# Kernel tuning notes

Measured on AMD Instinct MI355X. Metric: run time of the kernel, lower is better.

The kernel has to match this reference:

```python
import jax, jax.numpy as jnp
import numpy as np

N = 100000
D = 64
FE = 8
E = 1600000


def setup_inputs() -> dict:
    key = jax.random.key(0)
    ks = jax.random.split(key, 24)
    s = 0.05
    inp = {
        "H_adapted_t": jax.random.normal(ks[0], (N, D), jnp.float32),
        "event_vector": jax.random.normal(ks[1], (N, FE), jnp.float32),
        "edge_index": jax.random.randint(ks[2], (2, E), 0, N, jnp.int32),
        # event encoder MLP
        "enc_W1": jax.random.normal(ks[3], (FE, D), jnp.float32) * s,
        "enc_b1": jnp.zeros((D,), jnp.float32),
        "enc_W2": jax.random.normal(ks[4], (D, D), jnp.float32) * s,
        "enc_b2": jnp.zeros((D,), jnp.float32),
        # GCNConv
        "gcn_W": jax.random.normal(ks[5], (D, D), jnp.float32) * s,
        "gcn_b": jnp.zeros((D,), jnp.float32),
        # GATConv (heads=1, concat=False)
        "gat_W": jax.random.normal(ks[6], (D, D), jnp.float32) * s,
        "gat_att_src": jax.random.normal(ks[7], (D,), jnp.float32) * s,
        "gat_att_dst": jax.random.normal(ks[8], (D,), jnp.float32) * s,
        "gat_b": jnp.zeros((D,), jnp.float32),
        # gate fusion
        "gate_W": jax.random.normal(ks[9], (2 * D, D), jnp.float32) * s,
        "gate_b": jnp.zeros((D,), jnp.float32),
        # residual decoder
        "res_W1": jax.random.normal(ks[10], (2 * D, D), jnp.float32) * s,
        "res_b1": jnp.zeros((D,), jnp.float32),
        "res_W2": jax.random.normal(ks[11], (D, D), jnp.float32) * s,
        "res_b2": jnp.zeros((D,), jnp.float32),
        # speed head
        "sp_W1": jax.random.normal(ks[12], (D, 32), jnp.float32) * s,
        "sp_b1": jnp.zeros((32,), jnp.float32),
        "sp_W2": jax.random.normal(ks[13], (32, 1), jnp.float32) * s,
        "sp_b2": jnp.zeros((1,), jnp.float32),
    }
    return inp


def _gcn(x, src, dst, W, b, n):
    # PyG GCNConv: x' = D^{-1/2} (A + I) D^{-1/2} X W + b
    h = x @ W
    deg = jax.ops.segment_sum(jnp.ones_like(dst, jnp.float32), dst, num_segments=n)
    dinv = jnp.where(deg > 0, jax.lax.rsqrt(jnp.maximum(deg, 1e-12)), 0.0)
    norm = dinv[src] * dinv[dst]  # [E+N]
    out = jax.ops.segment_sum(h[src] * norm[:, None], dst, num_segments=n)
    return out + b


def _gat(x, src, dst, W, att_src, att_dst, b, n):
    # PyG GATConv (1 head): alpha = softmax_dst(leaky_relu(a_s.Wx_src + a_d.Wx_dst))
    h = x @ W
    a_s = h @ att_src  # [n]
    a_d = h @ att_dst
    e = jax.nn.leaky_relu(a_s[src] + a_d[dst], negative_slope=0.2)  # [E+N]
    m = jax.ops.segment_max(e, dst, num_segments=n)
    ex = jnp.exp(e - m[dst])
    z = jax.ops.segment_sum(ex, dst, num_segments=n)
    alpha = ex / z[dst]
    out = jax.ops.segment_sum(h[src] * alpha[:, None], dst, num_segments=n)
    return out + b


def reference(H_adapted_t, event_vector, edge_index,
              enc_W1, enc_b1, enc_W2, enc_b2,
              gcn_W, gcn_b,
              gat_W, gat_att_src, gat_att_dst, gat_b,
              gate_W, gate_b,
              res_W1, res_b1, res_W2, res_b2,
              sp_W1, sp_b1, sp_W2, sp_b2):
    n = H_adapted_t.shape[0]
    # add self-loops (PyG default for both convs)
    loop = jnp.arange(n, dtype=edge_index.dtype)
    src = jnp.concatenate([edge_index[0], loop])
    dst = jnp.concatenate([edge_index[1], loop])

    # event encoder
    emb = jax.nn.relu(event_vector @ enc_W1 + enc_b1) @ enc_W2 + enc_b2
    # diffusion: GCN -> ReLU -> GAT -> ReLU
    x = jax.nn.relu(_gcn(emb, src, dst, gcn_W, gcn_b, n))
    diffused = jax.nn.relu(_gat(x, src, dst, gat_W, gat_att_src, gat_att_dst, gat_b, n))

    fusion = jnp.concatenate([H_adapted_t, diffused], axis=-1)  # [N, 2D]
    gate = jax.nn.sigmoid(fusion @ gate_W + gate_b)
    delta_raw = jax.nn.relu(fusion @ res_W1 + res_b1) @ res_W2 + res_b2
    delta = gate * delta_raw
    H_final = H_adapted_t + delta
    pred_speed = (jax.nn.relu(H_final @ sp_W1 + sp_b1) @ sp_W2 + sp_b2)[:, 0]
    return (delta, H_final, pred_speed)
```

## Files before the change

kernel.cpp:

```cpp
#include <hip/hip_runtime.h>
#include <hip/hip_bf16.h>

#define NN 100000
#define DD 64
#define FEE 8
#define EE 1600000

#define NBUCK 391
#define BCAP 6144
#define CHA 4096
#define NBLKA ((EE + CHA - 1) / CHA)

typedef __attribute__((ext_vector_type(8))) short bf16x8;
typedef __attribute__((ext_vector_type(4))) float f32x4;
typedef __attribute__((ext_vector_type(2))) float f32x2;

__device__ __forceinline__ float b2f(unsigned short u) {
    return __uint_as_float(((unsigned)u) << 16);
}
__device__ __forceinline__ unsigned short f2b(float f) {
    unsigned u = __float_as_uint(f);
    unsigned r = 0x7fffu + ((u >> 16) & 1u);
    return (unsigned short)((u + r) >> 16);
}
__device__ __forceinline__ float lrelu(float v) { return v > 0.f ? v : 0.2f * v; }
__device__ __forceinline__ unsigned fkey(float x) {
    unsigned b = __float_as_uint(x);
    return (b & 0x80000000u) ? ~b : (b | 0x80000000u);
}
__device__ __forceinline__ float funkey(unsigned u) {
    unsigned b = (u & 0x80000000u) ? (u & 0x7fffffffu) : ~u;
    return __uint_as_float(b);
}
__device__ __forceinline__ bf16x8 pack8(const float* p) {
    const float4 a = *(const float4*)p;
    const float4 b = *(const float4*)(p + 4);
    bf16x8 r;
    r[0] = (short)f2b(a.x); r[1] = (short)f2b(a.y);
    r[2] = (short)f2b(a.z); r[3] = (short)f2b(a.w);
    r[4] = (short)f2b(b.x); r[5] = (short)f2b(b.y);
    r[6] = (short)f2b(b.z); r[7] = (short)f2b(b.w);
    return r;
}

__device__ __forceinline__ float deq8(unsigned v) {
#if __has_builtin(__builtin_amdgcn_cvt_f32_fp8)
    return __builtin_amdgcn_cvt_f32_fp8(v & 0xffu, 0);
#else
    unsigned t = v & 0x7fu;
    float m = __uint_as_float(0x3C000000u + (t << 20));
    if (t < 8) m = 2.f * m - 0.015625f;
    return (v & 0x80u) ? -m : m;
#endif
}
__device__ __forceinline__ float4 deq8x4(unsigned v) {
#if __has_builtin(__builtin_amdgcn_cvt_pk_f32_fp8)
    f32x2 lo = __builtin_amdgcn_cvt_pk_f32_fp8((int)v, false);
    f32x2 hi = __builtin_amdgcn_cvt_pk_f32_fp8((int)v, true);
    return make_float4(lo[0], lo[1], hi[0], hi[1]);
#else
    return make_float4(deq8(v), deq8(v >> 8), deq8(v >> 16), deq8(v >> 24));
#endif
}
__device__ __forceinline__ unsigned q8(float f) {
    unsigned u = __float_as_uint(f);
    unsigned s = (u >> 24) & 0x80u;
    float a = fminf(__uint_as_float(u & 0x7fffffffu), 448.f);
    unsigned t;
    if (a < 0.015625f) {
        t = (unsigned)__float2int_rn(a * 512.f);
    } else {
        unsigned b = __float_as_uint(a);
        b += ((b >> 20) & 1u) + 0x7FFFFu;
        unsigned e = (b >> 23) - 120u;
        t = (e > 15u) ? 0x7Eu : (((b >> 20) & 7u) | (e << 3));
    }
    return s | t;
}
__device__ __forceinline__ unsigned pk4(float a, float b, float c, float d) {
    return q8(a) | (q8(b) << 8) | (q8(c) << 16) | (q8(d) << 24);
}

#define LK 136
#define LK2 72

__global__ __launch_bounds__(256, 4) void k_encoder_mfma(
    const float* __restrict__ ev, const float* __restrict__ W1, const float* __restrict__ b1,
    const float* __restrict__ W2, const float* __restrict__ b2,
    const float* __restrict__ gcnW, const float* __restrict__ dinv,
    unsigned char* __restrict__ hA8)
{
    __shared__ short sW1T[64 * 32];
    __shared__ short sW2T[64 * LK2];
    __shared__ short sGWT[64 * LK2];
    __shared__ float sb1[64], sb2[64];
    __shared__ short sStage[4][16 * LK2];

    for (int t = threadIdx.x; t < 64 * 32; t += 256) {
        int n = t >> 5, k = t & 31;
        sW1T[n * 32 + k] = (k < FEE) ? (short)f2b(W1[k * 64 + n]) : (short)0;
    }
    for (int t = threadIdx.x; t < 64 * 64; t += 256) {
        int k = t >> 6, n = t & 63;
        sW2T[n * LK2 + k] = (short)f2b(W2[t]);
        sGWT[n * LK2 + k] = (short)f2b(gcnW[t]);
    }
    if (threadIdx.x < 64) {
        sb1[threadIdx.x] = b1[threadIdx.x];
        sb2[threadIdx.x] = b2[threadIdx.x];
    }
    __syncthreads();

    const int wave = threadIdx.x >> 6;
    const int lane = threadIdx.x & 63;
    const int m16  = lane & 15;
    const int quad = lane >> 4;
    short* myStage = &sStage[wave][0];

    const int ngroups = NN / 16;
    for (int g = blockIdx.x * 4 + wave; g < ngroups; g += gridDim.x * 4) {
        const int row0 = g * 16;
        bf16x8 a0;
        #pragma unroll
        for (int i = 0; i < 8; i++) a0[i] = 0;
        if (quad == 0) a0 = pack8(ev + (size_t)(row0 + m16) * FEE);
        f32x4 acc[4];
        #pragma unroll
        for (int c = 0; c < 4; c++) {
            f32x4 z = {0.f, 0.f, 0.f, 0.f};
            acc[c] = __builtin_amdgcn_mfma_f32_16x16x32_bf16(
                a0, *(const bf16x8*)&sW1T[(c * 16 + m16) * 32 + quad * 8], z, 0, 0, 0);
        }
        #pragma unroll
        for (int c = 0; c < 4; c++) {
            int n = c * 16 + m16;
            float bb = sb1[n];
            #pragma unroll
            for (int r = 0; r < 4; r++)
                myStage[(quad * 4 + r) * LK2 + n] = (short)f2b(fmaxf(acc[c][r] + bb, 0.f));
        }
        bf16x8 af0 = *(const bf16x8*)&myStage[m16 * LK2 + quad * 8];
        bf16x8 af1 = *(const bf16x8*)&myStage[m16 * LK2 + 32 + quad * 8];
        #pragma unroll
        for (int c = 0; c < 4; c++) {
            f32x4 z = {0.f, 0.f, 0.f, 0.f};
            const short* bp = &sW2T[(c * 16 + m16) * LK2 + quad * 8];
            z = __builtin_amdgcn_mfma_f32_16x16x32_bf16(af0, *(const bf16x8*)bp, z, 0, 0, 0);
            acc[c] = __builtin_amdgcn_mfma_f32_16x16x32_bf16(af1, *(const bf16x8*)(bp + 32), z, 0, 0, 0);
        }
        #pragma unroll
        for (int c = 0; c < 4; c++) {
            int n = c * 16 + m16;
            float bb = sb2[n];
            #pragma unroll
            for (int r = 0; r < 4; r++)
                myStage[(quad * 4 + r) * LK2 + n] = (short)f2b(acc[c][r] + bb);
        }
        af0 = *(const bf16x8*)&myStage[m16 * LK2 + quad * 8];
        af1 = *(const bf16x8*)&myStage[m16 * LK2 + 32 + quad * 8];
        #pragma unroll
        for (int c = 0; c < 4; c++) {
            f32x4 z = {0.f, 0.f, 0.f, 0.f};
            const short* bp = &sGWT[(c * 16 + m16) * LK2 + quad * 8];
            z = __builtin_amdgcn_mfma_f32_16x16x32_bf16(af0, *(const bf16x8*)bp, z, 0, 0, 0);
            acc[c] = __builtin_amdgcn_mfma_f32_16x16x32_bf16(af1, *(const bf16x8*)(bp + 32), z, 0, 0, 0);
        }
        #pragma unroll
        for (int c = 0; c < 4; c++) {
            int n = c * 16 + m16;
            #pragma unroll
            for (int r = 0; r < 4; r++)
                myStage[(quad * 4 + r) * LK2 + n] = (short)f2b(acc[c][r]);
        }
        #pragma unroll
        for (int h = 0; h < 2; h++) {
            int row = h * 8 + (lane >> 3);
            int col = (lane & 7) * 8;
            float sc = 32.f * dinv[row0 + row];
            const short* sp = &myStage[row * LK2 + col];
            uint2 w;
            w.x = pk4(b2f(sp[0]) * sc, b2f(sp[1]) * sc, b2f(sp[2]) * sc, b2f(sp[3]) * sc);
            w.y = pk4(b2f(sp[4]) * sc, b2f(sp[5]) * sc, b2f(sp[6]) * sc, b2f(sp[7]) * sc);
            *(uint2*)(hA8 + (size_t)(row0 + row) * 64 + col) = w;
        }
    }
}

__global__ __launch_bounds__(256, 4) void k_gatw_mfma(
    const unsigned short* __restrict__ x, const float* __restrict__ gatW,
    const float* __restrict__ attS, const float* __restrict__ attD,
    unsigned char* __restrict__ hC8, float* __restrict__ a_s, float* __restrict__ a_d)
{
    __shared__ short sGWT[64 * LK2];
    __shared__ float sAS[64], sAD[64];
    __shared__ short sStage[4][16 * LK2];
    for (int t = threadIdx.x; t < 64 * 64; t += 256) {
        int k = t >> 6, n = t & 63;
        sGWT[n * LK2 + k] = (short)f2b(gatW[t]);
    }
    if (threadIdx.x < 64) {
        sAS[threadIdx.x] = attS[threadIdx.x];
        sAD[threadIdx.x] = attD[threadIdx.x];
    }
    __syncthreads();

    const int wave = threadIdx.x >> 6;
    const int lane = threadIdx.x & 63;
    const int m16  = lane & 15;
    const int quad = lane >> 4;
    short* myStage = &sStage[wave][0];

    const int ngroups = NN / 16;
    for (int g = blockIdx.x * 4 + wave; g < ngroups; g += gridDim.x * 4) {
        const int row0 = g * 16;
        const unsigned short* xr = x + (size_t)(row0 + m16) * 64 + quad * 8;
        bf16x8 af0 = *(const bf16x8*)xr;
        bf16x8 af1 = *(const bf16x8*)(xr + 32);
        f32x4 acc[4];
        #pragma unroll
        for (int c = 0; c < 4; c++) {
            f32x4 z = {0.f, 0.f, 0.f, 0.f};
            const short* bp = &sGWT[(c * 16 + m16) * LK2 + quad * 8];
            z = __builtin_amdgcn_mfma_f32_16x16x32_bf16(af0, *(const bf16x8*)bp, z, 0, 0, 0);
            acc[c] = __builtin_amdgcn_mfma_f32_16x16x32_bf16(af1, *(const bf16x8*)(bp + 32), z, 0, 0, 0);
        }
        float ps[4] = {0.f, 0.f, 0.f, 0.f}, pd[4] = {0.f, 0.f, 0.f, 0.f};
        #pragma unroll
        for (int c = 0; c < 4; c++) {
            int n = c * 16 + m16;
            float was = sAS[n], wad = sAD[n];
            #pragma unroll
            for (int r = 0; r < 4; r++) {
                float v = acc[c][r];
                myStage[(quad * 4 + r) * LK2 + n] = (short)f2b(v);
                ps[r] += v * was;
                pd[r] += v * wad;
            }
        }
        #pragma unroll
        for (int off = 1; off < 16; off <<= 1) {
            #pragma unroll
            for (int r = 0; r < 4; r++) {
                ps[r] += __shfl_xor(ps[r], off, 64);
                pd[r] += __shfl_xor(pd[r], off, 64);
            }
        }
        if (m16 == 0) {
            #pragma unroll
            for (int r = 0; r < 4; r++) {
                a_s[row0 + quad * 4 + r] = ps[r];
                a_d[row0 + quad * 4 + r] = pd[r];
            }
        }
        #pragma unroll
        for (int h = 0; h < 2; h++) {
            int row = h * 8 + (lane >> 3);
            int col = (lane & 7) * 8;
            const short* sp = &myStage[row * LK2 + col];
            uint2 w;
            w.x = pk4(b2f(sp[0]) * 32.f, b2f(sp[1]) * 32.f, b2f(sp[2]) * 32.f, b2f(sp[3]) * 32.f);
            w.y = pk4(b2f(sp[4]) * 32.f, b2f(sp[5]) * 32.f, b2f(sp[6]) * 32.f, b2f(sp[7]) * 32.f);
            *(uint2*)(hC8 + (size_t)(row0 + row) * 64 + col) = w;
        }
    }
}

__global__ __launch_bounds__(512, 4) void k_decoder_mfma(
    const float* __restrict__ H, const float* diff,
    const float* __restrict__ gateW, const float* __restrict__ gateB,
    const float* __restrict__ resW1, const float* __restrict__ resB1,
    const float* __restrict__ resW2, const float* __restrict__ resB2,
    const float* __restrict__ spW1, const float* __restrict__ spB1,
    const float* __restrict__ spW2, const float* __restrict__ spB2,
    float* outDelta, float* __restrict__ outH, float* __restrict__ outP)
{
    __shared__ short sGW[64 * LK];
    __shared__ short sRW1[64 * LK];
    __shared__ short sRW2[64 * LK2];
    __shared__ short sSW1[32 * LK2];
    __shared__ float sGB[64], sRB1[64], sRB2[64];
    __shared__ float sSB1[32], sSW2[32];
    __shared__ float sSB2;
    __shared__ short sStage[8][16 * LK2];

    for (int t = threadIdx.x; t < 128 * 64; t += 512) {
        int k = t >> 6, n = t & 63;
        sGW[n * LK + k]  = (short)f2b(gateW[t]);
        sRW1[n * LK + k] = (short)f2b(resW1[t]);
    }
    for (int t = threadIdx.x; t < 64 * 64; t += 512) {
        int k = t >> 6, n = t & 63;
        sRW2[n * LK2 + k] = (short)f2b(resW2[t]);
    }
    for (int t = threadIdx.x; t < 64 * 32; t += 512) {
        int k = t >> 5, n = t & 31;
        sSW1[n * LK2 + k] = (short)f2b(spW1[t]);
    }
    if (threadIdx.x < 64) {
        sGB[threadIdx.x]  = gateB[threadIdx.x];
        sRB1[threadIdx.x] = resB1[threadIdx.x];
        sRB2[threadIdx.x] = resB2[threadIdx.x];
    }
    if (threadIdx.x < 32) {
        sSB1[threadIdx.x] = spB1[threadIdx.x];
        sSW2[threadIdx.x] = spW2[threadIdx.x];
    }
    if (threadIdx.x == 0) sSB2 = spB2[0];
    __syncthreads();

    const int wave = threadIdx.x >> 6;
    const int lane = threadIdx.x & 63;
    const int m16  = lane & 15;
    const int quad = lane >> 4;
    short* myStage = &sStage[wave][0];

    const int ngroups = NN / 16;
    for (int g = blockIdx.x * 8 + wave; g < ngroups; g += gridDim.x * 8) {
        const int row0 = g * 16;
        const float* Hrow = H    + (size_t)(row0 + m16) * 64 + quad * 8;
        const float* Drow = diff + (size_t)(row0 + m16) * 64 + quad * 8;
        bf16x8 afrag[4];
        afrag[0] = pack8(Hrow);
        afrag[1] = pack8(Hrow + 32);
        afrag[2] = pack8(Drow);
        afrag[3] = pack8(Drow + 32);

        f32x4 accG[4], accR[4];
        #pragma unroll
        for (int c = 0; c < 4; c++) {
            f32x4 z = {0.f, 0.f, 0.f, 0.f};
            accG[c] = z; accR[c] = z;
        }
        #pragma unroll
        for (int c = 0; c < 4; c++) {
            const short* bg = &sGW[(c * 16 + m16) * LK + quad * 8];
            const short* br = &sRW1[(c * 16 + m16) * LK + quad * 8];
            #pragma unroll
            for (int t = 0; t < 4; t++) {
                bf16x8 bgf = *(const bf16x8*)(bg + 32 * t);
                accG[c] = __builtin_amdgcn_mfma_f32_16x16x32_bf16(afrag[t], bgf, accG[c], 0, 0, 0);
                bf16x8 brf = *(const bf16x8*)(br + 32 * t);
                accR[c] = __builtin_amdgcn_mfma_f32_16x16x32_bf16(afrag[t], brf, accR[c], 0, 0, 0);
            }
        }

        float gateV[4][4];
        #pragma unroll
        for (int c = 0; c < 4; c++) {
            int n = c * 16 + m16;
            float gb = sGB[n], rb = sRB1[n];
            #pragma unroll
            for (int r = 0; r < 4; r++) {
                gateV[c][r] = 1.f / (1.f + __expf(-(accG[c][r] + gb)));
                int mrow = quad * 4 + r;
                myStage[mrow * LK2 + n] = (short)f2b(fmaxf(accR[c][r] + rb, 0.f));
            }
        }
        bf16x8 h1f0 = *(const bf16x8*)&myStage[m16 * LK2 + quad * 8];
        bf16x8 h1f1 = *(const bf16x8*)&myStage[m16 * LK2 + 32 + quad * 8];

        f32x4 accD[4];
        #pragma unroll
        for (int c = 0; c < 4; c++) { f32x4 z = {0.f, 0.f, 0.f, 0.f}; accD[c] = z; }
        #pragma unroll
        for (int c = 0; c < 4; c++) {
            const short* bp = &sRW2[(c * 16 + m16) * LK2 + quad * 8];
            accD[c] = __builtin_amdgcn_mfma_f32_16x16x32_bf16(h1f0, *(const bf16x8*)bp, accD[c], 0, 0, 0);
            accD[c] = __builtin_amdgcn_mfma_f32_16x16x32_bf16(h1f1, *(const bf16x8*)(bp + 32), accD[c], 0, 0, 0);
        }

        #pragma unroll
        for (int c = 0; c < 4; c++) {
            int n = c * 16 + m16;
            float rb2 = sRB2[n];
            #pragma unroll
            for (int r = 0; r < 4; r++) {
                int mrow = quad * 4 + r;
                float delta = gateV[c][r] * (accD[c][r] + rb2);
                float hv = H[(size_t)(row0 + mrow) * 64 + n];
                float hf = hv + delta;
                outDelta[(size_t)(row0 + mrow) * 64 + n] = delta;
                outH[(size_t)(row0 + mrow) * 64 + n] = hf;
                myStage[mrow * LK2 + n] = (short)f2b(hf);
            }
        }
        bf16x8 hff0 = *(const bf16x8*)&myStage[m16 * LK2 + quad * 8];
        bf16x8 hff1 = *(const bf16x8*)&myStage[m16 * LK2 + 32 + quad * 8];

        f32x4 accS[2];
        { f32x4 z = {0.f, 0.f, 0.f, 0.f}; accS[0] = z; accS[1] = z; }
        #pragma unroll
        for (int c = 0; c < 2; c++) {
            const short* bp = &sSW1[(c * 16 + m16) * LK2 + quad * 8];
            accS[c] = __builtin_amdgcn_mfma_f32_16x16x32_bf16(hff0, *(const bf16x8*)bp, accS[c], 0, 0, 0);
            accS[c] = __builtin_amdgcn_mfma_f32_16x16x32_bf16(hff1, *(const bf16x8*)(bp + 32), accS[c], 0, 0, 0);
        }
        float part[4];
        #pragma unroll
        for (int r = 0; r < 4; r++) {
            float p0 = fmaxf(accS[0][r] + sSB1[m16], 0.f) * sSW2[m16];
            float p1 = fmaxf(accS[1][r] + sSB1[16 + m16], 0.f) * sSW2[16 + m16];
            part[r] = p0 + p1;
        }
        #pragma unroll
        for (int off = 1; off < 16; off <<= 1) {
            #pragma unroll
            for (int r = 0; r < 4; r++) part[r] += __shfl_xor(part[r], off, 64);
        }
        if (m16 == 0) {
            #pragma unroll
            for (int r = 0; r < 4; r++) outP[row0 + quad * 4 + r] = part[r] + sSB2;
        }
    }
}


__global__ __launch_bounds__(256, 2) void k_binA(
    const int* __restrict__ src, const int* __restrict__ dst,
    int* __restrict__ bcnt, int* __restrict__ bpacked)
{
    __shared__ int sCount[512];
    __shared__ int sOff[512];
    __shared__ int sCur[512];
    __shared__ int sGbase[512];
    __shared__ int sWred[4];
    __shared__ int sStage[CHA];
    __shared__ unsigned short sBkt[CHA];
    const int t = threadIdx.x;
    const int e0 = blockIdx.x * CHA;
    const int len = min(CHA, EE - e0);

    for (int i = t; i < 512; i += 256) sCount[i] = 0;
    __syncthreads();
    for (int i = t; i < len; i += 256) atomicAdd(&sCount[dst[e0 + i] >> 8], 1);
    __syncthreads();
    int a0 = sCount[2 * t], a1 = sCount[2 * t + 1];
    int pairsum = a0 + a1;
    int x = pairsum;
    #pragma unroll
    for (int o = 1; o < 64; o <<= 1) {
        int y = __shfl_up(x, o, 64);
        if ((t & 63) >= o) x += y;
    }
    if ((t & 63) == 63) sWred[t >> 6] = x;
    __syncthreads();
    {
        int wid = t >> 6;
        int wbase = 0;
        if (wid > 0) wbase += sWred[0];
        if (wid > 1) wbase += sWred[1];
        if (wid > 2) wbase += sWred[2];
        x += wbase;
    }
    int excl = x - pairsum;
    sOff[2 * t] = excl;       sOff[2 * t + 1] = excl + a0;
    sCur[2 * t] = excl;       sCur[2 * t + 1] = excl + a0;
    __syncthreads();
    for (int b = t; b < NBUCK; b += 256) {
        int c = sCount[b];
        sGbase[b] = c ? atomicAdd(&bcnt[b], c) : 0;
    }
    __syncthreads();
    for (int i = t; i < len; i += 256) {
        int d = dst[e0 + i];
        int s = src[e0 + i];
        int b = d >> 8;
        int p = atomicAdd(&sCur[b], 1);
        sStage[p] = ((d & 255) << 17) | s;
        sBkt[p] = (unsigned short)b;
    }
    __syncthreads();
    for (int i = t; i < len; i += 256) {
        int b = sBkt[i];
        int gp = sGbase[b] + (i - sOff[b]);
        if (gp < BCAP) bpacked[(size_t)b * BCAP + gp] = sStage[i];
    }
}

__global__ __launch_bounds__(256) void k_fillB2(
    const int* __restrict__ bcnt, const int* __restrict__ bpacked,
    int* __restrict__ row_ptr, int* __restrict__ rend, float* __restrict__ dinv,
    int* __restrict__ csr)
{
    __shared__ int lcnt[256];
    __shared__ int lcur[256];
    __shared__ int lstage[BCAP];
    __shared__ int sWs[4];
    __shared__ int sWred[4];
    __shared__ int sBase;
    const int b = blockIdx.x;
    const int t = threadIdx.x;
    const int node0 = b << 8;
    const int cnt = min(bcnt[b], BCAP);
    lcnt[t] = 0;
    int partial = 0;
    for (int i = t; i < b; i += 256) partial += bcnt[i];
    #pragma unroll
    for (int o = 32; o >= 1; o >>= 1) partial += __shfl_xor(partial, o, 64);
    if ((t & 63) == 0) sWs[t >> 6] = partial;
    __syncthreads();
    if (t == 0) sBase = sWs[0] + sWs[1] + sWs[2] + sWs[3];
    const int* bp = bpacked + (size_t)b * BCAP;
    for (int i = t; i < cnt; i += 256) atomicAdd(&lcnt[bp[i] >> 17], 1);
    __syncthreads();
    const int base = sBase;
    int own = lcnt[t];
    int x = own;
    #pragma unroll
    for (int o = 1; o < 64; o <<= 1) {
        int y = __shfl_up(x, o, 64);
        if ((t & 63) >= o) x += y;
    }
    if ((t & 63) == 63) sWred[t >> 6] = x;
    __syncthreads();
    {
        int wid = t >> 6;
        int wbase = 0;
        if (wid > 0) wbase += sWred[0];
        if (wid > 1) wbase += sWred[1];
        if (wid > 2) wbase += sWred[2];
        x += wbase;
    }
    int excl = x - own;
    int node = node0 + t;
    if (node < NN) {
        row_ptr[node] = base + excl;
        rend[node] = base + excl + own;
        dinv[node] = rsqrtf((float)own + 1.0f);
    }
    lcur[t] = excl;
    __syncthreads();
    for (int i = t; i < cnt; i += 256) {
        int v = bp[i];
        int p = atomicAdd(&lcur[v >> 17], 1);
        lstage[p] = v & 0x1FFFF;
    }
    __syncthreads();
    for (int i = t; i < cnt; i += 256) csr[base + i] = lstage[i];
}


__global__ __launch_bounds__(256) void k_gcn_gather(
    const int* __restrict__ row_ptr, const int* __restrict__ rend,
    const int* __restrict__ csr, const float* __restrict__ dinv,
    const unsigned char* __restrict__ hA8, const float* __restrict__ gcnB,
    unsigned short* __restrict__ x)
{
    __shared__ int2 sE[4][4][16];
    const int wave = threadIdx.x >> 6;
    const int lane = threadIdx.x & 63;
    const int q    = lane >> 4;
    const int hl   = lane & 15;
    const int c4   = hl * 4;
    int2* myE = sE[wave][q];
    const float4 gb = *(const float4*)(gcnB + c4);
    const int stride = gridDim.x * 16;
    for (int node = blockIdx.x * 16 + wave * 4 + q; node < NN; node += stride) {
        const int base = row_ptr[node], end = rend[node];
        float r0 = 0.f, r1 = 0.f, r2 = 0.f, r3 = 0.f;
        for (int cb = base; cb < end; cb += 16) {
            int rem = end - cb; if (rem > 16) rem = 16;
            int sidx = 0; float w = 0.f;
            if (hl < rem) { sidx = csr[cb + hl]; w = 1.f; }
            myE[hl] = make_int2(sidx, __float_as_int(w));
            if (rem == 16) {
                unsigned vv[16]; float ww[16];
                #pragma unroll
                for (int j = 0; j < 16; j++) {
                    int2 e = myE[j];
                    ww[j] = __int_as_float(e.y);
                    vv[j] = *(const unsigned*)(hA8 + (((unsigned)e.x << 6) | (unsigned)c4));
                }
                #pragma unroll
                for (int j = 0; j < 16; j++) {
                    float4 d = deq8x4(vv[j]);
                    r0 = fmaf(d.x, ww[j], r0); r1 = fmaf(d.y, ww[j], r1);
                    r2 = fmaf(d.z, ww[j], r2); r3 = fmaf(d.w, ww[j], r3);
                }
            } else {
                for (int k = 0; k < rem; k += 8) {
                    unsigned vv[8]; float ww[8];
                    #pragma unroll
                    for (int j = 0; j < 8; j++) {
                        int2 e = myE[k + j];
                        ww[j] = __int_as_float(e.y);
                        vv[j] = *(const unsigned*)(hA8 + (((unsigned)e.x << 6) | (unsigned)c4));
                    }
                    #pragma unroll
                    for (int j = 0; j < 8; j++) {
                        float4 d = deq8x4(vv[j]);
                        r0 = fmaf(d.x, ww[j], r0); r1 = fmaf(d.y, ww[j], r1);
                        r2 = fmaf(d.z, ww[j], r2); r3 = fmaf(d.w, ww[j], r3);
                    }
                }
            }
        }
        unsigned sv = *(const unsigned*)(hA8 + (((unsigned)node << 6) | (unsigned)c4));
        float4 sd = deq8x4(sv);
        float sc = dinv[node] * 0.03125f;
        float o0 = fmaxf(fmaf(r0 + sd.x, sc, gb.x), 0.f);
        float o1 = fmaxf(fmaf(r1 + sd.y, sc, gb.y), 0.f);
        float o2 = fmaxf(fmaf(r2 + sd.z, sc, gb.z), 0.f);
        float o3 = fmaxf(fmaf(r3 + sd.w, sc, gb.w), 0.f);
        uint2 wv;
        wv.x = (unsigned)f2b(o0) | ((unsigned)f2b(o1) << 16);
        wv.y = (unsigned)f2b(o2) | ((unsigned)f2b(o3) << 16);
        *(uint2*)(x + (size_t)node * 64 + c4) = wv;
    }
}

__global__ __launch_bounds__(256) void k_gat_fused(
    const int* __restrict__ row_ptr, const int* __restrict__ rend,
    const int* __restrict__ csr,
    const float* __restrict__ a_s, const float* __restrict__ a_d,
    const unsigned char* __restrict__ hC8, const float* __restrict__ gatB,
    float* __restrict__ diff)
{
    __shared__ int2 sE[4][4][16];
    const int wave = threadIdx.x >> 6;
    const int lane = threadIdx.x & 63;
    const int q    = lane >> 4;
    const int hl   = lane & 15;
    const int c4   = hl * 4;
    int2* myE = sE[wave][q];
    const float4 gb = *(const float4*)(gatB + c4);
    const int stride = gridDim.x * 16;
    for (int node = blockIdx.x * 16 + wave * 4 + q; node < NN; node += stride) {
        const int base = row_ptr[node], end = rend[node];
        const float adn = a_d[node];
        const float p0 = __expf(lrelu(a_s[node] + adn));
        float zl = 0.f;
        float r0 = 0.f, r1 = 0.f, r2 = 0.f, r3 = 0.f;
        for (int cb = base; cb < end; cb += 16) {
            int rem = end - cb; if (rem > 16) rem = 16;
            int sidx = 0; float p = 0.f;
            if (hl < rem) {
                sidx = csr[cb + hl];
                p = __expf(lrelu(a_s[sidx] + adn));
            }
            myE[hl] = make_int2(sidx, __float_as_int(p));
            zl += p;
            if (rem == 16) {
                unsigned vv[16]; float ww[16];
                #pragma unroll
                for (int j = 0; j < 16; j++) {
                    int2 e = myE[j];
                    ww[j] = __int_as_float(e.y);
                    vv[j] = *(const unsigned*)(hC8 + (((unsigned)e.x << 6) | (unsigned)c4));
                }
                #pragma unroll
                for (int j = 0; j < 16; j++) {
                    float4 d = deq8x4(vv[j]);
                    r0 = fmaf(d.x, ww[j], r0); r1 = fmaf(d.y, ww[j], r1);
                    r2 = fmaf(d.z, ww[j], r2); r3 = fmaf(d.w, ww[j], r3);
                }
            } else {
                for (int k = 0; k < rem; k += 8) {
                    unsigned vv[8]; float ww[8];
                    #pragma unroll
                    for (int j = 0; j < 8; j++) {
                        int2 e = myE[k + j];
                        ww[j] = __int_as_float(e.y);
                        vv[j] = *(const unsigned*)(hC8 + (((unsigned)e.x << 6) | (unsigned)c4));
                    }
                    #pragma unroll
                    for (int j = 0; j < 8; j++) {
                        float4 d = deq8x4(vv[j]);
                        r0 = fmaf(d.x, ww[j], r0); r1 = fmaf(d.y, ww[j], r1);
                        r2 = fmaf(d.z, ww[j], r2); r3 = fmaf(d.w, ww[j], r3);
                    }
                }
            }
        }
        zl += __shfl_xor(zl, 1, 64);
        zl += __shfl_xor(zl, 2, 64);
        zl += __shfl_xor(zl, 4, 64);
        zl += __shfl_xor(zl, 8, 64);
        float z = p0 + zl;
        unsigned sv = *(const unsigned*)(hC8 + (((unsigned)node << 6) | (unsigned)c4));
        float4 sd = deq8x4(sv);
        r0 = fmaf(sd.x, p0, r0); r1 = fmaf(sd.y, p0, r1);
        r2 = fmaf(sd.z, p0, r2); r3 = fmaf(sd.w, p0, r3);
        float inv = 1.f / (32.f * z);
        float4 ov;
        ov.x = fmaxf(fmaf(r0, inv, gb.x), 0.f);
        ov.y = fmaxf(fmaf(r1, inv, gb.y), 0.f);
        ov.z = fmaxf(fmaf(r2, inv, gb.z), 0.f);
        ov.w = fmaxf(fmaf(r3, inv, gb.w), 0.f);
        *(float4*)(diff + (size_t)node * 64 + c4) = ov;
    }
}


__global__ __launch_bounds__(256, 4) void k_encoder(
    const float* __restrict__ ev, const float* __restrict__ W1, const float* __restrict__ b1,
    const float* __restrict__ W2, const float* __restrict__ b2,
    const float* __restrict__ gcnW, unsigned short* __restrict__ hA)
{
    __shared__ float sW1[FEE * DD];
    __shared__ float sW2[DD * DD];
    __shared__ float sGW[DD * DD];
    __shared__ float sb1[DD], sb2[DD];
    __shared__ float stage[4 * DD];
    for (int t = threadIdx.x; t < FEE * DD; t += 256) sW1[t] = W1[t];
    for (int t = threadIdx.x; t < DD * DD; t += 256) sW2[t] = W2[t];
    for (int t = threadIdx.x; t < DD * DD; t += 256) sGW[t] = gcnW[t];
    if (threadIdx.x < DD) {
        sb1[threadIdx.x] = b1[threadIdx.x];
        sb2[threadIdx.x] = b2[threadIdx.x];
    }
    __syncthreads();
    const int slot = threadIdx.x >> 6, j = threadIdx.x & 63;
    const int ngroups = NN / 4;
    for (int g = blockIdx.x; g < ngroups; g += gridDim.x) {
        int node = g * 4 + slot;
        const float* evp = ev + node * FEE;
        float accv = sb1[j];
        #pragma unroll
        for (int i = 0; i < FEE; i++) accv += evp[i] * sW1[i * DD + j];
        float hid = fmaxf(accv, 0.f);
        stage[slot * DD + j] = hid;
        __syncthreads();
        float embv = sb2[j];
        #pragma unroll 8
        for (int i = 0; i < DD; i++) embv += stage[slot * DD + i] * sW2[i * DD + j];
        __syncthreads();
        stage[slot * DD + j] = embv;
        __syncthreads();
        float hv = 0.f;
        #pragma unroll 8
        for (int i = 0; i < DD; i++) hv += stage[slot * DD + i] * sGW[i * DD + j];
        hA[node * DD + j] = f2b(hv);
        __syncthreads();
    }
}

__global__ void k_degf(const int* __restrict__ dst, float* __restrict__ deg) {
    int e = blockIdx.x * 256 + threadIdx.x;
    if (e < EE) atomicAdd(&deg[dst[e]], 1.0f);
}
__global__ void k_dinvf(float* deg) {
    int i = blockIdx.x * 256 + threadIdx.x;
    if (i < NN) deg[i] = rsqrtf(deg[i] + 1.0f);
}
__global__ __launch_bounds__(256) void k_gcn_agg(
    const int* __restrict__ src, const int* __restrict__ dst,
    const float* __restrict__ dinv, const unsigned short* __restrict__ hA,
    float* __restrict__ acc)
{
    int lane = threadIdx.x & 63;
    int w = blockIdx.x * 4 + (threadIdx.x >> 6);
    int nw = gridDim.x * 4;
    for (int e = w; e < EE; e += nw) {
        int s = src[e], d = dst[e];
        float norm = dinv[s] * dinv[d];
        atomicAdd(&acc[d * DD + lane], b2f(hA[s * DD + lane]) * norm);
    }
}
__global__ __launch_bounds__(256, 4) void k_gcn_post(
    const float* __restrict__ acc, const unsigned short* __restrict__ hA,
    const float* __restrict__ dinv, const float* __restrict__ gcnB,
    const float* __restrict__ gatW, const float* __restrict__ attS, const float* __restrict__ attD,
    unsigned short* __restrict__ hC, float* __restrict__ a_s, float* __restrict__ a_d,
    unsigned int* __restrict__ mkey)
{
    __shared__ float sGW[DD * DD];
    __shared__ float sB[DD], sAS[DD], sAD[DD];
    __shared__ float stage[4 * DD];
    for (int t = threadIdx.x; t < DD * DD; t += 256) sGW[t] = gatW[t];
    if (threadIdx.x < DD) {
        sB[threadIdx.x] = gcnB[threadIdx.x];
        sAS[threadIdx.x] = attS[threadIdx.x];
        sAD[threadIdx.x] = attD[threadIdx.x];
    }
    __syncthreads();
    const int slot = threadIdx.x >> 6, j = threadIdx.x & 63;
    const int ngroups = NN / 4;
    for (int g = blockIdx.x; g < ngroups; g += gridDim.x) {
        int node = g * 4 + slot;
        float dv = dinv[node];
        float xv = fmaxf(acc[node * DD + j] + b2f(hA[node * DD + j]) * dv * dv + sB[j], 0.f);
        stage[slot * DD + j] = xv;
        __syncthreads();
        float hv = 0.f;
        #pragma unroll 8
        for (int i = 0; i < DD; i++) hv += stage[slot * DD + i] * sGW[i * DD + j];
        hC[node * DD + j] = f2b(hv);
        float ts = hv * sAS[j], td = hv * sAD[j];
        #pragma unroll
        for (int m = 32; m >= 1; m >>= 1) {
            ts += __shfl_xor(ts, m, 64);
            td += __shfl_xor(td, m, 64);
        }
        if (j == 0) {
            a_s[node] = ts;
            a_d[node] = td;
            mkey[node] = fkey(lrelu(ts + td));
        }
        __syncthreads();
    }
}
__global__ void k_gat_max(const int* __restrict__ src, const int* __restrict__ dst,
                          const float* __restrict__ a_s, const float* __restrict__ a_d,
                          unsigned int* __restrict__ mkey) {
    int e = blockIdx.x * 256 + threadIdx.x;
    if (e < EE) {
        int d = dst[e];
        float v = lrelu(a_s[src[e]] + a_d[d]);
        atomicMax(&mkey[d], fkey(v));
    }
}
__global__ void k_gat_mz(const float* __restrict__ a_s, const float* __restrict__ a_d,
                         unsigned int* __restrict__ mkey, float* __restrict__ z) {
    int i = blockIdx.x * 256 + threadIdx.x;
    if (i < NN) {
        float m = funkey(mkey[i]);
        float es = lrelu(a_s[i] + a_d[i]);
        z[i] = expf(es - m);
        ((float*)mkey)[i] = m;
    }
}
__global__ void k_gat_z(const int* __restrict__ src, const int* __restrict__ dst,
                        const float* __restrict__ a_s, const float* __restrict__ a_d,
                        const float* __restrict__ mf, float* __restrict__ z) {
    int e = blockIdx.x * 256 + threadIdx.x;
    if (e < EE) {
        int d = dst[e];
        float v = lrelu(a_s[src[e]] + a_d[d]);
        atomicAdd(&z[d], expf(v - mf[d]));
    }
}
__global__ __launch_bounds__(256) void k_gat_agg(
    const int* __restrict__ src, const int* __restrict__ dst,
    const float* __restrict__ a_s, const float* __restrict__ a_d,
    const float* __restrict__ mf, const float* __restrict__ z,
    const unsigned short* __restrict__ hC, float* __restrict__ acc)
{
    int lane = threadIdx.x & 63;
    int w = blockIdx.x * 4 + (threadIdx.x >> 6);
    int nw = gridDim.x * 4;
    for (int e = w; e < EE; e += nw) {
        int s = src[e], d = dst[e];
        float v = lrelu(a_s[s] + a_d[d]);
        float alpha = expf(v - mf[d]) / z[d];
        atomicAdd(&acc[d * DD + lane], b2f(hC[s * DD + lane]) * alpha);
    }
}
__global__ void k_gat_post(float* __restrict__ acc, const unsigned short* __restrict__ hC,
                           const float* __restrict__ a_s, const float* __restrict__ a_d,
                           const float* __restrict__ mf, const float* __restrict__ z,
                           const float* __restrict__ gatB) {
    int idx = blockIdx.x * 256 + threadIdx.x;
    if (idx < NN * DD) {
        int i = idx >> 6, j = idx & 63;
        float es = lrelu(a_s[i] + a_d[i]);
        float sw = expf(es - mf[i]) / z[i];
        float v = acc[idx] + sw * b2f(hC[idx]) + gatB[j];
        acc[idx] = fmaxf(v, 0.f);
    }
}


extern "C" void kernel_launch(void* const* d_in, const int* in_sizes, int n_in,
                              void* d_out, int out_size, void* d_ws, size_t ws_size,
                              hipStream_t stream) {
    const float* H     = (const float*)d_in[0];
    const float* ev    = (const float*)d_in[1];
    const int*   ei    = (const int*)d_in[2];
    const float* encW1 = (const float*)d_in[3];
    const float* encB1 = (const float*)d_in[4];
    const float* encW2 = (const float*)d_in[5];
    const float* encB2 = (const float*)d_in[6];
    const float* gcnW  = (const float*)d_in[7];
    const float* gcnB  = (const float*)d_in[8];
    const float* gatW  = (const float*)d_in[9];
    const float* attS  = (const float*)d_in[10];
    const float* attD  = (const float*)d_in[11];
    const float* gatB  = (const float*)d_in[12];
    const float* gateW = (const float*)d_in[13];
    const float* gateB = (const float*)d_in[14];
    const float* resW1 = (const float*)d_in[15];
    const float* resB1 = (const float*)d_in[16];
    const float* resW2 = (const float*)d_in[17];
    const float* resB2 = (const float*)d_in[18];
    const float* spW1  = (const float*)d_in[19];
    const float* spB1  = (const float*)d_in[20];
    const float* spW2  = (const float*)d_in[21];
    const float* spB2  = (const float*)d_in[22];

    const int* srcI = ei;
    const int* dstI = ei + EE;

    float* outDelta = (float*)d_out;
    float* outH     = outDelta + (size_t)NN * DD;
    float* outP     = outH + (size_t)NN * DD;

    float* diff = outDelta;
    int* bpacked = (int*)outDelta;
    unsigned short* x   = (unsigned short*)outDelta;
    unsigned char* hA8  = (unsigned char*)outH;
    unsigned char* hC8  = hA8 + (size_t)NN * DD;

    const size_t csr_need = ((size_t)4 * NN + EE + 1024) * 4;

    if (ws_size >= csr_need) {
        float* dinv = (float*)d_ws;
        float* a_s  = dinv + NN;
        float* a_d  = a_s + NN;
        int* rend   = (int*)(a_d + NN);
        int* csr    = rend + NN;
        int* bcntg  = csr + EE;
        int* row_ptr = (int*)outP;

        hipMemsetAsync(bcntg, 0, (size_t)512 * 4, stream);
        k_binA<<<NBLKA, 256, 0, stream>>>(srcI, dstI, bcntg, bpacked);
        k_fillB2<<<NBUCK, 256, 0, stream>>>(bcntg, bpacked,
                                            row_ptr, rend, dinv, csr);
        k_encoder_mfma<<<1024, 256, 0, stream>>>(ev, encW1, encB1, encW2, encB2,
                                                 gcnW, dinv, hA8);
        k_gcn_gather<<<4096, 256, 0, stream>>>(row_ptr, rend, csr, dinv, hA8, gcnB, x);
        k_gatw_mfma<<<1024, 256, 0, stream>>>(x, gatW, attS, attD, hC8, a_s, a_d);
        k_gat_fused<<<4096, 256, 0, stream>>>(row_ptr, rend, csr, a_s, a_d, hC8, gatB, diff);
    } else {
        float* dinv = (float*)d_ws;
        float* a_s  = dinv + NN;
        float* a_d  = a_s + NN;
        float* mf   = a_d + NN;
        float* z    = mf + NN;
        float* acc  = diff;
        unsigned short* hA = (unsigned short*)outH;
        unsigned short* hC = hA + (size_t)NN * DD;

        hipMemsetAsync(dinv, 0, (size_t)NN * 4, stream);
        hipMemsetAsync(acc, 0, (size_t)NN * DD * 4, stream);
        k_encoder<<<1024, 256, 0, stream>>>(ev, encW1, encB1, encW2, encB2, gcnW, hA);
        k_degf<<<(EE + 255) / 256, 256, 0, stream>>>(dstI, dinv);
        k_dinvf<<<(NN + 255) / 256, 256, 0, stream>>>(dinv);
        k_gcn_agg<<<8192, 256, 0, stream>>>(srcI, dstI, dinv, hA, acc);
        k_gcn_post<<<1024, 256, 0, stream>>>(acc, hA, dinv, gcnB, gatW, attS, attD,
                                             hC, a_s, a_d, (unsigned int*)mf);
        hipMemsetAsync(acc, 0, (size_t)NN * DD * 4, stream);
        k_gat_max<<<(EE + 255) / 256, 256, 0, stream>>>(srcI, dstI, a_s, a_d, (unsigned int*)mf);
        k_gat_mz<<<(NN + 255) / 256, 256, 0, stream>>>(a_s, a_d, (unsigned int*)mf, z);
        k_gat_z<<<(EE + 255) / 256, 256, 0, stream>>>(srcI, dstI, a_s, a_d, mf, z);
        k_gat_agg<<<8192, 256, 0, stream>>>(srcI, dstI, a_s, a_d, mf, z, hC, acc);
        k_gat_post<<<(NN * DD) / 256, 256, 0, stream>>>(acc, hC, a_s, a_d, mf, z, gatB);
    }

    k_decoder_mfma<<<512, 512, 0, stream>>>(H, diff, gateW, gateB, resW1, resB1,
                                            resW2, resB2, spW1, spB1, spW2, spB2,
                                            outDelta, outH, outP);
}
```

Baseline: 257.7 us.

## Split fp8 feature tables into column halves and gather each half separately

```diff
diff --git a/kernel.cpp b/kernel.cpp
--- a/kernel.cpp
+++ b/kernel.cpp
@@ -88,7 +88,7 @@
     const float* __restrict__ ev, const float* __restrict__ W1, const float* __restrict__ b1,
     const float* __restrict__ W2, const float* __restrict__ b2,
     const float* __restrict__ gcnW, const float* __restrict__ dinv,
-    unsigned char* __restrict__ hA8)
+    unsigned char* __restrict__ hA8lo, unsigned char* __restrict__ hA8hi)
 {
     __shared__ short sW1T[64 * 32];
     __shared__ short sW2T[64 * LK2];
@@ -181,7 +181,10 @@
             uint2 w;
             w.x = pk4(b2f(sp[0]) * sc, b2f(sp[1]) * sc, b2f(sp[2]) * sc, b2f(sp[3]) * sc);
             w.y = pk4(b2f(sp[4]) * sc, b2f(sp[5]) * sc, b2f(sp[6]) * sc, b2f(sp[7]) * sc);
-            *(uint2*)(hA8 + (size_t)(row0 + row) * 64 + col) = w;
+            unsigned char* dst = (col < 32)
+                ? hA8lo + (size_t)(row0 + row) * 32 + col
+                : hA8hi + (size_t)(row0 + row) * 32 + (col - 32);
+            *(uint2*)dst = w;
         }
     }
 }
@@ -189,7 +192,8 @@
 __global__ __launch_bounds__(256, 4) void k_gatw_mfma(
     const unsigned short* __restrict__ x, const float* __restrict__ gatW,
     const float* __restrict__ attS, const float* __restrict__ attD,
-    unsigned char* __restrict__ hC8, float* __restrict__ a_s, float* __restrict__ a_d)
+    unsigned char* __restrict__ hC8lo, unsigned char* __restrict__ hC8hi,
+    float* __restrict__ a_s, float* __restrict__ a_d)
 {
     __shared__ short sGWT[64 * LK2];
     __shared__ float sAS[64], sAD[64];
@@ -260,7 +264,10 @@
             uint2 w;
             w.x = pk4(b2f(sp[0]) * 32.f, b2f(sp[1]) * 32.f, b2f(sp[2]) * 32.f, b2f(sp[3]) * 32.f);
             w.y = pk4(b2f(sp[4]) * 32.f, b2f(sp[5]) * 32.f, b2f(sp[6]) * 32.f, b2f(sp[7]) * 32.f);
-            *(uint2*)(hC8 + (size_t)(row0 + row) * 64 + col) = w;
+            unsigned char* dst = (col < 32)
+                ? hC8lo + (size_t)(row0 + row) * 32 + col
+                : hC8hi + (size_t)(row0 + row) * 32 + (col - 32);
+            *(uint2*)dst = w;
         }
     }
 }
@@ -543,33 +550,35 @@
 __global__ __launch_bounds__(256) void k_gcn_gather(
     const int* __restrict__ row_ptr, const int* __restrict__ rend,
     const int* __restrict__ csr, const float* __restrict__ dinv,
-    const unsigned char* __restrict__ hA8, const float* __restrict__ gcnB,
-    unsigned short* __restrict__ x)
-{
-    __shared__ int2 sE[4][4][16];
+    const unsigned char* __restrict__ tab, const float* __restrict__ gcnB,
+    int colbase, unsigned short* __restrict__ x)
+{
+    __shared__ int2 sE[4][8][16];
     const int wave = threadIdx.x >> 6;
     const int lane = threadIdx.x & 63;
-    const int q    = lane >> 4;
-    const int hl   = lane & 15;
+    const int q    = lane >> 3;
+    const int hl   = lane & 7;
     const int c4   = hl * 4;
     int2* myE = sE[wave][q];
-    const float4 gb = *(const float4*)(gcnB + c4);
-    const int stride = gridDim.x * 16;
-    for (int node = blockIdx.x * 16 + wave * 4 + q; node < NN; node += stride) {
+    const float4 gb = *(const float4*)(gcnB + colbase + c4);
+    const int stride = gridDim.x * 32;
+    for (int node = blockIdx.x * 32 + wave * 8 + q; node < NN; node += stride) {
         const int base = row_ptr[node], end = rend[node];
         float r0 = 0.f, r1 = 0.f, r2 = 0.f, r3 = 0.f;
         for (int cb = base; cb < end; cb += 16) {
             int rem = end - cb; if (rem > 16) rem = 16;
-            int sidx = 0; float w = 0.f;
-            if (hl < rem) { sidx = csr[cb + hl]; w = 1.f; }
-            myE[hl] = make_int2(sidx, __float_as_int(w));
+            int s0 = 0, s1 = 0; float w0 = 0.f, w1 = 0.f;
+            if (hl < rem)     { s0 = csr[cb + hl];     w0 = 1.f; }
+            if (hl + 8 < rem) { s1 = csr[cb + 8 + hl]; w1 = 1.f; }
+            myE[hl]     = make_int2(s0, __float_as_int(w0));
+            myE[hl + 8] = make_int2(s1, __float_as_int(w1));
             if (rem == 16) {
                 unsigned vv[16]; float ww[16];
                 #pragma unroll
                 for (int j = 0; j < 16; j++) {
                     int2 e = myE[j];
                     ww[j] = __int_as_float(e.y);
-                    vv[j] = *(const unsigned*)(hA8 + (((unsigned)e.x << 6) | (unsigned)c4));
+                    vv[j] = *(const unsigned*)(tab + (((unsigned)e.x << 5) | (unsigned)c4));
                 }
                 #pragma unroll
                 for (int j = 0; j < 16; j++) {
@@ -584,7 +593,7 @@
                     for (int j = 0; j < 8; j++) {
                         int2 e = myE[k + j];
                         ww[j] = __int_as_float(e.y);
-                        vv[j] = *(const unsigned*)(hA8 + (((unsigned)e.x << 6) | (unsigned)c4));
+                        vv[j] = *(const unsigned*)(tab + (((unsigned)e.x << 5) | (unsigned)c4));
                     }
                     #pragma unroll
                     for (int j = 0; j < 8; j++) {
@@ -595,7 +604,7 @@
                 }
             }
         }
-        unsigned sv = *(const unsigned*)(hA8 + (((unsigned)node << 6) | (unsigned)c4));
+        unsigned sv = *(const unsigned*)(tab + (((unsigned)node << 5) | (unsigned)c4));
         float4 sd = deq8x4(sv);
         float sc = dinv[node] * 0.03125f;
         float o0 = fmaxf(fmaf(r0 + sd.x, sc, gb.x), 0.f);
@@ -605,7 +614,7 @@
         uint2 wv;
         wv.x = (unsigned)f2b(o0) | ((unsigned)f2b(o1) << 16);
         wv.y = (unsigned)f2b(o2) | ((unsigned)f2b(o3) << 16);
-        *(uint2*)(x + (size_t)node * 64 + c4) = wv;
+        *(uint2*)(x + (size_t)node * 64 + colbase + c4) = wv;
     }
 }
 
@@ -613,19 +622,19 @@
     const int* __restrict__ row_ptr, const int* __restrict__ rend,
     const int* __restrict__ csr,
     const float* __restrict__ a_s, const float* __restrict__ a_d,
-    const unsigned char* __restrict__ hC8, const float* __restrict__ gatB,
-    float* __restrict__ diff)
-{
-    __shared__ int2 sE[4][4][16];
+    const unsigned char* __restrict__ tab, const float* __restrict__ gatB,
+    int colbase, float* __restrict__ diff)
+{
+    __shared__ int2 sE[4][8][16];
     const int wave = threadIdx.x >> 6;
     const int lane = threadIdx.x & 63;
-    const int q    = lane >> 4;
-    const int hl   = lane & 15;
+    const int q    = lane >> 3;
+    const int hl   = lane & 7;
     const int c4   = hl * 4;
     int2* myE = sE[wave][q];
-    const float4 gb = *(const float4*)(gatB + c4);
-    const int stride = gridDim.x * 16;
-    for (int node = blockIdx.x * 16 + wave * 4 + q; node < NN; node += stride) {
+    const float4 gb = *(const float4*)(gatB + colbase + c4);
+    const int stride = gridDim.x * 32;
+    for (int node = blockIdx.x * 32 + wave * 8 + q; node < NN; node += stride) {
         const int base = row_ptr[node], end = rend[node];
         const float adn = a_d[node];
         const float p0 = __expf(lrelu(a_s[node] + adn));
@@ -633,20 +642,25 @@
         float r0 = 0.f, r1 = 0.f, r2 = 0.f, r3 = 0.f;
         for (int cb = base; cb < end; cb += 16) {
             int rem = end - cb; if (rem > 16) rem = 16;
-            int sidx = 0; float p = 0.f;
+            int s0 = 0, s1 = 0; float p0e = 0.f, p1e = 0.f;
             if (hl < rem) {
-                sidx = csr[cb + hl];
-                p = __expf(lrelu(a_s[sidx] + adn));
+                s0 = csr[cb + hl];
+                p0e = __expf(lrelu(a_s[s0] + adn));
             }
-            myE[hl] = make_int2(sidx, __float_as_int(p));
-            zl += p;
+            if (hl + 8 < rem) {
+                s1 = csr[cb + 8 + hl];
+                p1e = __expf(lrelu(a_s[s1] + adn));
+            }
+            myE[hl]     = make_int2(s0, __float_as_int(p0e));
+            myE[hl + 8] = make_int2(s1, __float_as_int(p1e));
+            zl += p0e + p1e;
             if (rem == 16) {
                 unsigned vv[16]; float ww[16];
                 #pragma unroll
                 for (int j = 0; j < 16; j++) {
                     int2 e = myE[j];
                     ww[j] = __int_as_float(e.y);
-                    vv[j] = *(const unsigned*)(hC8 + (((unsigned)e.x << 6) | (unsigned)c4));
+                    vv[j] = *(const unsigned*)(tab + (((unsigned)e.x << 5) | (unsigned)c4));
                 }
                 #pragma unroll
                 for (int j = 0; j < 16; j++) {
@@ -661,7 +675,7 @@
                     for (int j = 0; j < 8; j++) {
                         int2 e = myE[k + j];
                         ww[j] = __int_as_float(e.y);
-                        vv[j] = *(const unsigned*)(hC8 + (((unsigned)e.x << 6) | (unsigned)c4));
+                        vv[j] = *(const unsigned*)(tab + (((unsigned)e.x << 5) | (unsigned)c4));
                     }
                     #pragma unroll
                     for (int j = 0; j < 8; j++) {
@@ -675,9 +689,8 @@
         zl += __shfl_xor(zl, 1, 64);
         zl += __shfl_xor(zl, 2, 64);
         zl += __shfl_xor(zl, 4, 64);
-        zl += __shfl_xor(zl, 8, 64);
         float z = p0 + zl;
-        unsigned sv = *(const unsigned*)(hC8 + (((unsigned)node << 6) | (unsigned)c4));
+        unsigned sv = *(const unsigned*)(tab + (((unsigned)node << 5) | (unsigned)c4));
         float4 sd = deq8x4(sv);
         r0 = fmaf(sd.x, p0, r0); r1 = fmaf(sd.y, p0, r1);
         r2 = fmaf(sd.z, p0, r2); r3 = fmaf(sd.w, p0, r3);
@@ -687,7 +700,7 @@
         ov.y = fmaxf(fmaf(r1, inv, gb.y), 0.f);
         ov.z = fmaxf(fmaf(r2, inv, gb.z), 0.f);
         ov.w = fmaxf(fmaf(r3, inv, gb.w), 0.f);
-        *(float4*)(diff + (size_t)node * 64 + c4) = ov;
+        *(float4*)(diff + (size_t)node * 64 + colbase + c4) = ov;
     }
 }
 
@@ -897,9 +910,11 @@
 
     float* diff = outDelta;
     int* bpacked = (int*)outDelta;
-    unsigned short* x   = (unsigned short*)outDelta;
-    unsigned char* hA8  = (unsigned char*)outH;
-    unsigned char* hC8  = hA8 + (size_t)NN * DD;
+    unsigned short* x    = (unsigned short*)outDelta;
+    unsigned char* hA8lo = (unsigned char*)outH;
+    unsigned char* hA8hi = hA8lo + (size_t)NN * 32;
+    unsigned char* hC8lo = hA8hi + (size_t)NN * 32;
+    unsigned char* hC8hi = hC8lo + (size_t)NN * 32;
 
     const size_t csr_need = ((size_t)4 * NN + EE + 1024) * 4;
 
@@ -917,10 +932,17 @@
         k_fillB2<<<NBUCK, 256, 0, stream>>>(bcntg, bpacked,
                                             row_ptr, rend, dinv, csr);
         k_encoder_mfma<<<1024, 256, 0, stream>>>(ev, encW1, encB1, encW2, encB2,
-                                                 gcnW, dinv, hA8);
-        k_gcn_gather<<<4096, 256, 0, stream>>>(row_ptr, rend, csr, dinv, hA8, gcnB, x);
-        k_gatw_mfma<<<1024, 256, 0, stream>>>(x, gatW, attS, attD, hC8, a_s, a_d);
-        k_gat_fused<<<4096, 256, 0, stream>>>(row_ptr, rend, csr, a_s, a_d, hC8, gatB, diff);
+                                                 gcnW, dinv, hA8lo, hA8hi);
+        k_gcn_gather<<<3125, 256, 0, stream>>>(row_ptr, rend, csr, dinv, hA8lo,
+                                               gcnB, 0, x);
+        k_gcn_gather<<<3125, 256, 0, stream>>>(row_ptr, rend, csr, dinv, hA8hi,
+                                               gcnB, 32, x);
+        k_gatw_mfma<<<1024, 256, 0, stream>>>(x, gatW, attS, attD,
+                                              hC8lo, hC8hi, a_s, a_d);
+        k_gat_fused<<<3125, 256, 0, stream>>>(row_ptr, rend, csr, a_s, a_d,
+                                              hC8lo, gatB, 0, diff);
+        k_gat_fused<<<3125, 256, 0, stream>>>(row_ptr, rend, csr, a_s, a_d,
+                                              hC8hi, gatB, 32, diff);
     } else {
         float* dinv = (float*)d_ws;
         float* a_s  = dinv + NN;
```

After: 284.9 us. 1.11x slower.
